# Kernel optimization log

Hardware: AMD Instinct MI355X
Metric: run time of the kernel (lower is better)

Reference implementation:

```python
import jax, jax.numpy as jnp
import numpy as np
import math

B, M, C = 4, 2048, 1024
H = 8
DQK = C // 4 // H   # 32
DV = C // H         # 128
LEAKY_SLOPE = 0.2


def setup_inputs() -> dict:
    key = jax.random.key(0)
    ks = jax.random.split(key, 9)
    s = 1.0 / math.sqrt(C)
    return {
        "x": jax.random.normal(ks[0], (B, M, C), jnp.float32),
        "y": jax.random.normal(ks[1], (B, M, C), jnp.float32),
        "Wq": jax.random.normal(ks[2], (C, C // 4), jnp.float32) * s,
        "bq": jax.random.normal(ks[3], (C // 4,), jnp.float32) * s,
        "Wk": jax.random.normal(ks[4], (C, C // 4), jnp.float32) * s,
        "bk": jax.random.normal(ks[5], (C // 4,), jnp.float32) * s,
        "Wv": jax.random.normal(ks[6], (C, C), jnp.float32) * s,
        "bv": jax.random.normal(ks[7], (C,), jnp.float32) * s,
        "gamma": jax.random.normal(ks[8], (1,), jnp.float32) * 0.1,
    }


def reference(x, y, Wq, bq, Wk, bk, Wv, bv, gamma):
    b, m, c = x.shape
    m2 = y.shape[1]
    # projections; split heads
    f = (x @ Wq + bq).reshape(b, m, H, DQK)    # queries
    g = (y @ Wk + bk).reshape(b, m2, H, DQK)   # keys
    h = (y @ Wv + bv).reshape(b, m2, H, DV)    # values
    scores = jnp.einsum('bmhd,bnhd->bhmn', f, g) / math.sqrt(DQK)
    scores = jnp.where(scores >= 0, scores, LEAKY_SLOPE * scores)  # leaky_relu(0.2)
    beta = jax.nn.softmax(scores, axis=-1)
    o = jnp.einsum('bhmn,bnhd->bmhd', beta, h)  # [B, M, H, DV]
    return gamma[0] * o.reshape(b, m, c) + x
```

## Files before the change

kernel.cpp:

```cpp
#include <hip/hip_runtime.h>
#include <cstdint>
#include <cstddef>

typedef unsigned short u16;
typedef unsigned int u32;
typedef __attribute__((ext_vector_type(8))) short bf16x8;
typedef __attribute__((ext_vector_type(4))) float f32x4;
typedef __attribute__((ext_vector_type(16))) float f32x16;

__device__ __forceinline__ u16 f2bf(float f) {
  union { float f; unsigned int u; } v; v.f = f;
  unsigned int r = v.u + 0x7fffu + ((v.u >> 16) & 1u);
  return (u16)(r >> 16);
}

__device__ __forceinline__ u32 pack_bf_trunc(float hi, float lo) {
#if __has_builtin(__builtin_amdgcn_perm)
  return __builtin_amdgcn_perm(__float_as_uint(hi), __float_as_uint(lo), 0x07060302u);
#else
  return (__float_as_uint(hi) & 0xffff0000u) | (__float_as_uint(lo) >> 16);
#endif
}

__device__ __forceinline__ void glds16(const void* g, void* l) {
  __builtin_amdgcn_global_load_lds(
      (const __attribute__((address_space(1))) unsigned int*)g,
      (__attribute__((address_space(3))) unsigned int*)l, 16, 0, 0);
}

__device__ __forceinline__ f32x4 fzero4() { f32x4 z = {0.f, 0.f, 0.f, 0.f}; return z; }
__device__ __forceinline__ f32x16 fzero16() {
  f32x16 z;
  #pragma unroll
  for (int i = 0; i < 16; ++i) z[i] = 0.f;
  return z;
}

__global__ __launch_bounds__(256)
void prep_kernel(const float* __restrict__ x, u16* __restrict__ xb,
                 const float* __restrict__ y, u16* __restrict__ yb,
                 const float* __restrict__ Wq, const float* __restrict__ Wk,
                 const float* __restrict__ Wv, u16* __restrict__ wt) {
  __shared__ float tile[32][33];
  int bx = blockIdx.x;
  if (bx < 2048) {
    #pragma unroll 2
    for (int i = bx * 256 + threadIdx.x; i < 4194304; i += 2048 * 256) {
      const float* src; u16* dst; int j = i;
      if (j < 2097152) { src = x; dst = xb; }
      else             { src = y; dst = yb; j -= 2097152; }
      float4 v = ((const float4*)src)[j];
      ((ushort4*)dst)[j] = make_ushort4(f2bf(v.x), f2bf(v.y), f2bf(v.z), f2bf(v.w));
    }
    return;
  }
  int tb = bx - 2048;
  for (int t = tb; t < 1536; t += 512) {
    const float* in; u16* out; int N, tn;
    if (t < 256)      { in = Wq; out = wt;              N = 256;  tn = t; }
    else if (t < 512) { in = Wk; out = wt + 256 * 1024; N = 256;  tn = t - 256; }
    else              { in = Wv; out = wt + 512 * 1024; N = 1024; tn = t - 512; }
    int ntiles = N >> 5;
    int n0 = (tn % ntiles) * 32, k0 = (tn / ntiles) * 32;
    int tx = threadIdx.x & 31, ty = threadIdx.x >> 5;
    __syncthreads();
    #pragma unroll
    for (int j = ty; j < 32; j += 8) tile[j][tx] = in[(size_t)(k0 + j) * N + n0 + tx];
    __syncthreads();
    #pragma unroll
    for (int j = ty; j < 32; j += 8) out[(size_t)(n0 + j) * 1024 + k0 + tx] = f2bf(tile[tx][j]);
  }
}

__global__ __launch_bounds__(256, 4)
void gemm_all_kernel(const u16* __restrict__ xb, const u16* __restrict__ yb,
                     const u16* __restrict__ wt,
                     const float* __restrict__ bq, const float* __restrict__ bk,
                     const float* __restrict__ bv,
                     u16* __restrict__ fb, u16* __restrict__ gb, u16* __restrict__ ht) {
  __shared__ __align__(16) u16 ls[17408];
  u16* lA = ls;
  u16* lB = ls + 8192;
  const int tid = threadIdx.x, lane = tid & 63;
  const int quad = lane >> 4, l16 = lane & 15;
  const int wave = tid >> 6;

  int lin = blockIdx.x + 12 * blockIdx.y;
  lin = (lin & 7) * 96 + (lin >> 3);
  const int col0 = (lin % 12) * 128, row0 = (lin / 12) * 128;

  const int wm = (wave >> 1) * 64, wn = (wave & 1) * 64;
  const u16* A = (col0 < 256) ? xb : yb;

  f32x4 acc[4][4];
  #pragma unroll
  for (int i = 0; i < 4; i++)
    #pragma unroll
    for (int j = 0; j < 4; j++) acc[i][j] = fzero4();

  for (int k0 = 0; k0 < 1024; k0 += 64) {
    __syncthreads();
    #pragma unroll
    for (int i = 0; i < 4; i++) {
      int c = i * 256 + tid;
      glds16(A + (size_t)(row0 + (c & 127)) * 1024 + k0 + (c >> 7) * 8, lA + c * 8);
    }
    #pragma unroll
    for (int i = 0; i < 4; i++) {
      int c = i * 256 + tid;
      glds16(wt + (size_t)(col0 + (c & 127)) * 1024 + k0 + (c >> 7) * 8, lB + c * 8);
    }
    __syncthreads();
    #pragma unroll
    for (int kk = 0; kk < 2; kk++) {
      bf16x8 af[4], bfr[4];
      #pragma unroll
      for (int mi = 0; mi < 4; mi++)
        af[mi] = *(const bf16x8*)(lA + ((kk * 4 + quad) * 128 + wm + mi * 16 + l16) * 8);
      #pragma unroll
      for (int ni = 0; ni < 4; ni++)
        bfr[ni] = *(const bf16x8*)(lB + ((kk * 4 + quad) * 128 + wn + ni * 16 + l16) * 8);
      #pragma unroll
      for (int mi = 0; mi < 4; mi++)
        #pragma unroll
        for (int ni = 0; ni < 4; ni++)
          acc[mi][ni] = __builtin_amdgcn_mfma_f32_16x16x32_bf16(af[mi], bfr[ni], acc[mi][ni], 0, 0, 0);
    }
  }

  if (col0 < 512) {
    #pragma unroll
    for (int mi = 0; mi < 4; mi++)
      #pragma unroll
      for (int ni = 0; ni < 4; ni++) {
        int col = col0 + wn + ni * 16 + l16;
        float bvv = (col < 256) ? bq[col] : bk[col - 256];
        #pragma unroll
        for (int r = 0; r < 4; r++) {
          int row = row0 + wm + mi * 16 + quad * 4 + r;
          float v = acc[mi][ni][r] + bvv;
          int bb = row >> 11, ml = row & 2047;
          if (col < 256) {
            int h = col >> 5, kk2 = col & 31;
            fb[(((size_t)(bb * 8 + h)) << 16) + ml * 32 + kk2] = f2bf(v);
          } else {
            int c2 = col - 256, h = c2 >> 5, kk2 = c2 & 31;
            gb[((((size_t)(bb * 8 + h)) * 16 + (ml >> 7)) << 12)
               + (kk2 >> 3) * 1024 + (ml & 127) * 8 + (kk2 & 7)] = f2bf(v);
          }
        }
      }
  } else {
    const int headblk = (col0 - 512) >> 7;
    const int bb = row0 >> 11, mloc0 = row0 & 2047;
    __syncthreads();
    #pragma unroll
    for (int mi = 0; mi < 4; mi++)
      #pragma unroll
      for (int ni = 0; ni < 4; ni++) {
        int col = wn + ni * 16 + l16;
        int rowl = wm + mi * 16 + quad * 4;
        float bvv = bv[(col0 - 512) + col];
        float v0 = acc[mi][ni][0] + bvv, v1 = acc[mi][ni][1] + bvv;
        float v2 = acc[mi][ni][2] + bvv, v3 = acc[mi][ni][3] + bvv;
        *(uint2*)(ls + col * 136 + rowl) =
            make_uint2(pack_bf_trunc(v1, v0), pack_bf_trunc(v3, v2));
      }
    __syncthreads();
    u16* tb = ht + ((((size_t)(bb * 8 + headblk)) * 16 + (mloc0 >> 7)) << 14);
    #pragma unroll
    for (int i = 0; i < 8; ++i) {
      int chunk = i * 256 + tid;
      *(uint4*)(tb + chunk * 8) = *(const uint4*)(ls + (chunk & 127) * 136 + (chunk >> 7) * 8);
    }
  }
}

__global__ __launch_bounds__(256, 2)
void attn_kernel(const u16* __restrict__ fb, const u16* __restrict__ gb,
                 const u16* __restrict__ ht, const float* __restrict__ x,
                 const float* __restrict__ gamma, float* __restrict__ out) {
  __shared__ __align__(16) u16 lK[2][4096];
  __shared__ __align__(16) u16 lV[2][16384];
  const int tid = threadIdx.x;
  const int lane = tid & 63, wave = tid >> 6;
  const int hd = lane >> 5, l31 = lane & 31;

  int lin = blockIdx.x + 16 * blockIdx.y + 128 * blockIdx.z;
  const int head = lin & 7;
  const int mblk = (lin >> 3) & 15;
  const int b = lin >> 7;
  const int m0 = mblk * 128;
  const int bh = b * 8 + head;

  const float sscale = 0.17677669529663687f * 1.4426950408889634f;

  const int qrow = m0 + wave * 32 + l31;
  union { bf16x8 v; u16 s[8]; } q0, q1;
  {
    const u16* qp = fb + (((size_t)bh * 2048 + qrow) << 5);
    q0.v = *(const bf16x8*)(qp + hd * 8);
    q1.v = *(const bf16x8*)(qp + 16 + hd * 8);
    #pragma unroll
    for (int j = 0; j < 8; ++j) {
      q0.s[j] = f2bf(__uint_as_float((u32)q0.s[j] << 16) * sscale);
      q1.s[j] = f2bf(__uint_as_float((u32)q1.s[j] << 16) * sscale);
    }
  }

  f32x16 oacc[4];
  #pragma unroll
  for (int i = 0; i < 4; ++i) oacc[i] = fzero16();
  float lsacc[4] = {0.f, 0.f, 0.f, 0.f};

  const u16* kbase = gb + ((size_t)bh << 16);
  const u16* vbase = ht + ((size_t)bh << 18);

  auto stage = [&](int bufsel, int nt) {
    const u16* ks_ = kbase + ((size_t)nt << 12);
    const u16* vs_ = vbase + ((size_t)nt << 14);
    #pragma unroll
    for (int i = 0; i < 2; ++i) glds16(ks_ + (i * 256 + tid) * 8, &lK[bufsel][(i * 256 + tid) * 8]);
    #pragma unroll
    for (int i = 0; i < 8; ++i) glds16(vs_ + (i * 256 + tid) * 8, &lV[bufsel][(i * 256 + tid) * 8]);
  };

  auto compute = [&](const u16* Kc, const u16* Vc) {
    u32 pk[4][8];
    #pragma unroll
    for (int nt4 = 0; nt4 < 4; ++nt4) {
      bf16x8 k0 = *(const bf16x8*)(Kc + hd * 1024 + (nt4 * 32 + l31) * 8);
      bf16x8 k1 = *(const bf16x8*)(Kc + (2 + hd) * 1024 + (nt4 * 32 + l31) * 8);
      __builtin_amdgcn_s_setprio(1);
      f32x16 s = __builtin_amdgcn_mfma_f32_32x32x16_bf16(k0, q0.v, fzero16(), 0, 0, 0);
      s = __builtin_amdgcn_mfma_f32_32x32x16_bf16(k1, q1.v, s, 0, 0, 0);
      __builtin_amdgcn_s_setprio(0);
      float p[16];
      #pragma unroll
      for (int r = 0; r < 16; ++r) {
        float sv = s[r];
        float lv = fmaxf(sv, 0.2f * sv);
        p[r] = __builtin_amdgcn_exp2f(lv);
        lsacc[r & 3] += p[r];
      }
      #pragma unroll
      for (int s2 = 0; s2 < 4; ++s2) {
        pk[nt4][s2 * 2 + 0] = pack_bf_trunc(p[s2 * 4 + 1], p[s2 * 4 + 0]);
        pk[nt4][s2 * 2 + 1] = pack_bf_trunc(p[s2 * 4 + 3], p[s2 * 4 + 2]);
      }
    }

    #pragma unroll
    for (int kt = 0; kt < 8; ++kt) {
      const int nt4 = kt >> 1, a = kt & 1;
      u32 w0 = pk[nt4][a * 4 + 0], w1 = pk[nt4][a * 4 + 1];
      u32 w2 = pk[nt4][a * 4 + 2], w3 = pk[nt4][a * 4 + 3];
      asm("v_permlane32_swap_b32 %0, %1" : "+v"(w0), "+v"(w2));
      asm("v_permlane32_swap_b32 %0, %1" : "+v"(w1), "+v"(w3));
      union { u32 w[4]; bf16x8 v; } pf;
      pf.w[0] = w0; pf.w[1] = w1; pf.w[2] = w2; pf.w[3] = w3;
      __builtin_amdgcn_s_setprio(1);
      #pragma unroll
      for (int dvt = 0; dvt < 4; ++dvt) {
        bf16x8 vf = *(const bf16x8*)(Vc + (kt * 2 + hd) * 1024 + (dvt * 32 + l31) * 8);
        oacc[dvt] = __builtin_amdgcn_mfma_f32_32x32x16_bf16(pf.v, vf, oacc[dvt], 0, 0, 0);
      }
      __builtin_amdgcn_s_setprio(0);
    }
  };

  stage(0, 0);
  __syncthreads();

  #pragma unroll 1
  for (int it = 0; it < 16; it += 2) {
    stage(1, it + 1);
    compute(&lK[0][0], &lV[0][0]);
    __syncthreads();
    if (it + 2 < 16) stage(0, it + 2);
    compute(&lK[1][0], &lV[1][0]);
    __syncthreads();
  }

  float lsum = (lsacc[0] + lsacc[1]) + (lsacc[2] + lsacc[3]);
  float ltot = lsum + __shfl_xor(lsum, 32, 64);
  float inv = 1.0f / ltot;
  const float gam = gamma[0];
  const size_t rowbase = ((size_t)(b * 2048 + m0 + wave * 32)) * 1024 + head * 128 + l31;
  #pragma unroll
  for (int reg = 0; reg < 16; ++reg) {
    const int m32 = (reg & 3) + 8 * (reg >> 2) + 4 * hd;
    float iv = __shfl(inv, m32, 64);
    #pragma unroll
    for (int dvt = 0; dvt < 4; ++dvt) {
      size_t idx = rowbase + (size_t)m32 * 1024 + dvt * 32;
      out[idx] = gam * (oacc[dvt][reg] * iv) + x[idx];
    }
  }
}

extern "C" void kernel_launch(void* const* d_in, const int* in_sizes, int n_in,
                              void* d_out, int out_size, void* d_ws, size_t ws_size,
                              hipStream_t stream) {
  const float* x     = (const float*)d_in[0];
  const float* y     = (const float*)d_in[1];
  const float* Wq    = (const float*)d_in[2];
  const float* bq    = (const float*)d_in[3];
  const float* Wk    = (const float*)d_in[4];
  const float* bk    = (const float*)d_in[5];
  const float* Wv    = (const float*)d_in[6];
  const float* bv    = (const float*)d_in[7];
  const float* gamma = (const float*)d_in[8];
  float* out = (float*)d_out;

  char* ws = (char*)d_ws;
  u16* xb = (u16*)(ws);
  u16* yb = (u16*)(ws + 16777216);
  u16* wt = (u16*)(ws + 33554432);
  u16* fb = (u16*)(ws + 36700160);
  u16* gb = (u16*)(ws + 40894464);
  u16* ht = (u16*)(ws + 45088768);

  prep_kernel<<<2560, 256, 0, stream>>>(x, xb, y, yb, Wq, Wk, Wv, wt);
  gemm_all_kernel<<<dim3(12, 64), 256, 0, stream>>>(xb, yb, wt, bq, bk, bv, fb, gb, ht);
  attn_kernel<<<dim3(16, 8, 4), 256, 0, stream>>>(fb, gb, ht, x, gamma, out);
}
```

Before: 237.8 us.

## Fuse fp32-to-bf16 activation conversion into GEMM A-tile loads

Removes the separate pass that converted x and y to bf16 workspace buffers. The GEMM now loads fp32 activations into registers, converts them with v_cvt_pk_bf16_f32 (round-to-nearest), and stores them to LDS with an XOR swizzle to avoid bank conflicts. This saves a full round trip of 32 MB of reads plus 16 MB of bf16 writes and re-reads. The trade-off is that each GEMM tile now reads A at fp32 width, twice the bytes, through registers rather than direct global-to-LDS loads, which adds register pressure and removes the async path for A.

```diff
diff --git a/kernel.cpp b/kernel.cpp
--- a/kernel.cpp
+++ b/kernel.cpp
@@ -22,6 +22,12 @@
 #endif
 }
 
+__device__ __forceinline__ u32 cvt_pk_bf16(float lo, float hi) {
+  u32 r;
+  asm("v_cvt_pk_bf16_f32 %0, %1, %2" : "=v"(r) : "v"(lo), "v"(hi));
+  return r;
+}
+
 __device__ __forceinline__ void glds16(const void* g, void* l) {
   __builtin_amdgcn_global_load_lds(
       (const __attribute__((address_space(1))) unsigned int*)g,
@@ -37,43 +43,26 @@
 }
 
 __global__ __launch_bounds__(256)
-void prep_kernel(const float* __restrict__ x, u16* __restrict__ xb,
-                 const float* __restrict__ y, u16* __restrict__ yb,
-                 const float* __restrict__ Wq, const float* __restrict__ Wk,
-                 const float* __restrict__ Wv, u16* __restrict__ wt) {
+void prep_w_kernel(const float* __restrict__ Wq, const float* __restrict__ Wk,
+                   const float* __restrict__ Wv, u16* __restrict__ wt) {
   __shared__ float tile[32][33];
-  int bx = blockIdx.x;
-  if (bx < 2048) {
-    #pragma unroll 2
-    for (int i = bx * 256 + threadIdx.x; i < 4194304; i += 2048 * 256) {
-      const float* src; u16* dst; int j = i;
-      if (j < 2097152) { src = x; dst = xb; }
-      else             { src = y; dst = yb; j -= 2097152; }
-      float4 v = ((const float4*)src)[j];
-      ((ushort4*)dst)[j] = make_ushort4(f2bf(v.x), f2bf(v.y), f2bf(v.z), f2bf(v.w));
-    }
-    return;
-  }
-  int tb = bx - 2048;
-  for (int t = tb; t < 1536; t += 512) {
-    const float* in; u16* out; int N, tn;
-    if (t < 256)      { in = Wq; out = wt;              N = 256;  tn = t; }
-    else if (t < 512) { in = Wk; out = wt + 256 * 1024; N = 256;  tn = t - 256; }
-    else              { in = Wv; out = wt + 512 * 1024; N = 1024; tn = t - 512; }
-    int ntiles = N >> 5;
-    int n0 = (tn % ntiles) * 32, k0 = (tn / ntiles) * 32;
-    int tx = threadIdx.x & 31, ty = threadIdx.x >> 5;
-    __syncthreads();
-    #pragma unroll
-    for (int j = ty; j < 32; j += 8) tile[j][tx] = in[(size_t)(k0 + j) * N + n0 + tx];
-    __syncthreads();
-    #pragma unroll
-    for (int j = ty; j < 32; j += 8) out[(size_t)(n0 + j) * 1024 + k0 + tx] = f2bf(tile[tx][j]);
-  }
+  int t = blockIdx.x;
+  const float* in; u16* out; int N, tn;
+  if (t < 256)      { in = Wq; out = wt;              N = 256;  tn = t; }
+  else if (t < 512) { in = Wk; out = wt + 256 * 1024; N = 256;  tn = t - 256; }
+  else              { in = Wv; out = wt + 512 * 1024; N = 1024; tn = t - 512; }
+  int ntiles = N >> 5;
+  int n0 = (tn % ntiles) * 32, k0 = (tn / ntiles) * 32;
+  int tx = threadIdx.x & 31, ty = threadIdx.x >> 5;
+  #pragma unroll
+  for (int j = ty; j < 32; j += 8) tile[j][tx] = in[(size_t)(k0 + j) * N + n0 + tx];
+  __syncthreads();
+  #pragma unroll
+  for (int j = ty; j < 32; j += 8) out[(size_t)(n0 + j) * 1024 + k0 + tx] = f2bf(tile[tx][j]);
 }
 
 __global__ __launch_bounds__(256, 4)
-void gemm_all_kernel(const u16* __restrict__ xb, const u16* __restrict__ yb,
+void gemm_all_kernel(const float* __restrict__ x, const float* __restrict__ y,
                      const u16* __restrict__ wt,
                      const float* __restrict__ bq, const float* __restrict__ bk,
                      const float* __restrict__ bv,
@@ -90,7 +79,7 @@
   const int col0 = (lin % 12) * 128, row0 = (lin / 12) * 128;
 
   const int wm = (wave >> 1) * 64, wn = (wave & 1) * 64;
-  const u16* A = (col0 < 256) ? xb : yb;
+  const float* Af = (col0 < 256) ? x : y;
 
   f32x4 acc[4][4];
   #pragma unroll
@@ -100,26 +89,41 @@
 
   for (int k0 = 0; k0 < 1024; k0 += 64) {
     __syncthreads();
+    float4 a[4][2];
     #pragma unroll
     for (int i = 0; i < 4; i++) {
       int c = i * 256 + tid;
-      glds16(A + (size_t)(row0 + (c & 127)) * 1024 + k0 + (c >> 7) * 8, lA + c * 8);
+      int row = c >> 3, kc = c & 7;
+      const float4* src = (const float4*)(Af + (size_t)(row0 + row) * 1024 + k0 + kc * 8);
+      a[i][0] = src[0];
+      a[i][1] = src[1];
     }
     #pragma unroll
     for (int i = 0; i < 4; i++) {
       int c = i * 256 + tid;
       glds16(wt + (size_t)(col0 + (c & 127)) * 1024 + k0 + (c >> 7) * 8, lB + c * 8);
     }
+    #pragma unroll
+    for (int i = 0; i < 4; i++) {
+      int c = i * 256 + tid;
+      int row = c >> 3, kc = c & 7;
+      u32 w0 = cvt_pk_bf16(a[i][0].x, a[i][0].y);
+      u32 w1 = cvt_pk_bf16(a[i][0].z, a[i][0].w);
+      u32 w2 = cvt_pk_bf16(a[i][1].x, a[i][1].y);
+      u32 w3 = cvt_pk_bf16(a[i][1].z, a[i][1].w);
+      *(uint4*)(lA + kc * 1024 + ((row ^ (kc << 1)) * 8)) = make_uint4(w0, w1, w2, w3);
+    }
     __syncthreads();
     #pragma unroll
     for (int kk = 0; kk < 2; kk++) {
       bf16x8 af[4], bfr[4];
+      const int kc = kk * 4 + quad;
       #pragma unroll
       for (int mi = 0; mi < 4; mi++)
-        af[mi] = *(const bf16x8*)(lA + ((kk * 4 + quad) * 128 + wm + mi * 16 + l16) * 8);
+        af[mi] = *(const bf16x8*)(lA + kc * 1024 + (((wm + mi * 16 + l16) ^ (kc << 1)) * 8));
       #pragma unroll
       for (int ni = 0; ni < 4; ni++)
-        bfr[ni] = *(const bf16x8*)(lB + ((kk * 4 + quad) * 128 + wn + ni * 16 + l16) * 8);
+        bfr[ni] = *(const bf16x8*)(lB + (kc * 128 + wn + ni * 16 + l16) * 8);
       #pragma unroll
       for (int mi = 0; mi < 4; mi++)
         #pragma unroll
@@ -314,14 +318,12 @@
   float* out = (float*)d_out;
 
   char* ws = (char*)d_ws;
-  u16* xb = (u16*)(ws);
-  u16* yb = (u16*)(ws + 16777216);
   u16* wt = (u16*)(ws + 33554432);
   u16* fb = (u16*)(ws + 36700160);
   u16* gb = (u16*)(ws + 40894464);
   u16* ht = (u16*)(ws + 45088768);
 
-  prep_kernel<<<2560, 256, 0, stream>>>(x, xb, y, yb, Wq, Wk, Wv, wt);
-  gemm_all_kernel<<<dim3(12, 64), 256, 0, stream>>>(xb, yb, wt, bq, bk, bv, fb, gb, ht);
+  prep_w_kernel<<<1536, 256, 0, stream>>>(Wq, Wk, Wv, wt);
+  gemm_all_kernel<<<dim3(12, 64), 256, 0, stream>>>(x, y, wt, bq, bk, bv, fb, gb, ht);
   attn_kernel<<<dim3(16, 8, 4), 256, 0, stream>>>(fb, gb, ht, x, gamma, out);
 }
```

Result: no change. 234.2 us (-1.5%).
